# Kernel tuning notes

Hardware: AMD Instinct MI355X
Metric: run time of the kernel (lower is better)

## Reference

```python
import jax, jax.numpy as jnp
import numpy as np
from jax import lax

C = 256        # shared head channels (out_ch)
NB = 6         # anchors per spatial location
NC = 9         # num_classes (incl. background)
B = 16         # batch
FM = [(38, 38), (19, 19), (10, 10), (5, 5), (3, 3), (1, 1)]
BIAS_PRIOR = -float(np.log((1.0 - 0.01) / 0.01))  # focal-style prior on cls bias


def _conv(x, w, b):
    # 3x3 conv, stride 1, SAME padding, NCHW/OIHW
    y = lax.conv_general_dilated(x, w, (1, 1), 'SAME',
                                 dimension_numbers=('NCHW', 'OIHW', 'NCHW'))
    return y + b[None, :, None, None]


def _head(x, ws, bs):
    for w, b in zip(ws[:-1], bs[:-1]):
        x = jax.nn.relu(_conv(x, w, b))
    return _conv(x, ws[-1], bs[-1])


def setup_inputs() -> dict:
    key = jax.random.key(0)
    ks = jax.random.split(key, 20)
    d = {}
    for i, (h, w) in enumerate(FM):
        d[f'feat{i}'] = jax.random.normal(ks[i], (B, C, h, w), dtype=jnp.float32)
    for i in range(4):
        d[f'rw{i}'] = 0.01 * jax.random.normal(ks[6 + i], (C, C, 3, 3), dtype=jnp.float32)
        d[f'rb{i}'] = jnp.zeros((C,), jnp.float32)
    d['rw4'] = 0.01 * jax.random.normal(ks[10], (NB * 4, C, 3, 3), dtype=jnp.float32)
    d['rb4'] = jnp.zeros((NB * 4,), jnp.float32)
    for i in range(4):
        d[f'cw{i}'] = 0.01 * jax.random.normal(ks[11 + i], (C, C, 3, 3), dtype=jnp.float32)
        d[f'cb{i}'] = jnp.zeros((C,), jnp.float32)
    d['cw4'] = 0.01 * jax.random.normal(ks[15], (NB * NC, C, 3, 3), dtype=jnp.float32)
    cb4 = jnp.zeros((NB * NC,), jnp.float32)
    d['cb4'] = cb4.at[:NB].set(BIAS_PRIOR)  # bias_per_class = n_boxes entries
    return d


def reference(feat0, feat1, feat2, feat3, feat4, feat5,
              rw0, rw1, rw2, rw3, rw4, rb0, rb1, rb2, rb3, rb4,
              cw0, cw1, cw2, cw3, cw4, cb0, cb1, cb2, cb3, cb4):
    feats = [feat0, feat1, feat2, feat3, feat4, feat5]
    rws = [rw0, rw1, rw2, rw3, rw4]
    rbs = [rb0, rb1, rb2, rb3, rb4]
    cws = [cw0, cw1, cw2, cw3, cw4]
    cbs = [cb0, cb1, cb2, cb3, cb4]
    locs, confs = [], []
    for x in feats:
        n = x.shape[0]
        locs.append(_head(x, rws, rbs).reshape(n, 4, -1))       # [N,4,NB*H*W]
        confs.append(_head(x, cws, cbs).reshape(n, NC, -1))     # [N,NC,NB*H*W]
    bbox_delta = jnp.concatenate(locs, axis=2)   # [N, 4, total_anchors]
    confidences = jnp.concatenate(confs, axis=2)  # [N, NC, total_anchors]
    return bbox_delta, confidences
```

## Files before the change

### kernel.cpp

```cpp
#include <hip/hip_runtime.h>
#include <hip/hip_bf16.h>

typedef __attribute__((ext_vector_type(8))) __bf16 bf16x8;
typedef __attribute__((ext_vector_type(4))) float f32x4;

__device__ __forceinline__ unsigned short f2bf(float f) {
    unsigned int u = __float_as_uint(f);
    u += 0x7fff + ((u >> 16) & 1);
    return (unsigned short)(u >> 16);
}

__device__ __forceinline__ void gload16(const void* g, void* l) {
    __builtin_amdgcn_global_load_lds(
        (const __attribute__((address_space(1))) void*)g,
        (__attribute__((address_space(3))) void*)l, 16, 0, 0);
}

#define ZOFFB (31040 * 512)

__device__ __forceinline__ void tile256(int rt, int& rb, int& dim, int& row0) {
    if (rt < 91)       { rb = 0;     dim = 38; row0 = rt * 256; }
    else if (rt < 114) { rb = 23104; dim = 19; row0 = (rt - 91) * 256; }
    else if (rt < 121) { rb = 28880; dim = 10; row0 = (rt - 114) * 256; }
    else if (rt < 123) { rb = 30480; dim = 5;  row0 = (rt - 121) * 256; }
    else if (rt < 124) { rb = 30880; dim = 3;  row0 = (rt - 123) * 256; }
    else               { rb = 31024; dim = 1;  row0 = 0; }
    row0 += rb;
}

__device__ __forceinline__ void tile128(int rt, int& rb, int& dim, int& row0, int& aoff) {
    if (rt < 181)      { rb = 0;     dim = 38; row0 = rt * 128;         aoff = 0;     }
    else if (rt < 227) { rb = 23104; dim = 19; row0 = (rt - 181) * 128; aoff = 8664;  }
    else if (rt < 240) { rb = 28880; dim = 10; row0 = (rt - 227) * 128; aoff = 10830; }
    else if (rt < 244) { rb = 30480; dim = 5;  row0 = (rt - 240) * 128; aoff = 11430; }
    else if (rt < 246) { rb = 30880; dim = 3;  row0 = (rt - 244) * 128; aoff = 11580; }
    else               { rb = 31024; dim = 1;  row0 = (rt - 246) * 128; aoff = 11634; }
    row0 += rb;
}

struct WT { const float* src[10]; };
__global__ void wtrans_all(WT wt, unsigned short* __restrict__ Wb, unsigned short* __restrict__ WF) {
    int idx = blockIdx.x * 256 + threadIdx.x;
    if (idx >= 5013504) return;
    const float* src;
    unsigned short* dst;
    int lo, Cout;
    if (idx < 4718592) {
        int slot = idx / 589824;
        lo = idx - slot * 589824;
        src = wt.src[slot];
        dst = Wb + (size_t)slot * 589824;
        Cout = 256;
    } else {
        int r = idx - 4718592;
        int slot = r / 147456;
        lo = r - slot * 147456;
        src = wt.src[8 + slot];
        dst = WF + (size_t)slot * 147456;
        Cout = slot ? 54 : 24;
    }
    int co = lo / 2304;
    int k  = lo - co * 2304;
    int tap = k >> 8;
    int ci  = k & 255;
    float v = (co < Cout) ? src[(co * 256 + ci) * 9 + tap] : 0.0f;
    dst[lo] = f2bf(v);
}

struct FT { const float* src[6]; unsigned short* halo[4]; int nh; };
__global__ void ftrans_all(FT ft, unsigned short* __restrict__ X0) {
    int idx = blockIdx.x * 256 + threadIdx.x;
    if (idx >= 993280) {
        int idx2 = idx - 993280;
        int buf = idx2 >> 8, off = idx2 & 255;
        if (buf < ft.nh) ft.halo[buf][off] = 0;
        return;
    }
    int row = idx >> 5;
    int c8  = (idx & 31) << 3;
    int m, rb, dim;
    if (row < 23104)      { m = 0; rb = 0;     dim = 38; }
    else if (row < 28880) { m = 1; rb = 23104; dim = 19; }
    else if (row < 30480) { m = 2; rb = 28880; dim = 10; }
    else if (row < 30880) { m = 3; rb = 30480; dim = 5;  }
    else if (row < 31024) { m = 4; rb = 30880; dim = 3;  }
    else                  { m = 5; rb = 31024; dim = 1;  }
    int HW = dim * dim;
    int rel = row - rb;
    int b = rel / HW;
    int hw = rel - b * HW;
    const float* s = ft.src[m] + (size_t)(b * 256 + c8) * HW + hw;
    union { unsigned short u[8]; uint4 v; } tmp;
#pragma unroll
    for (int j = 0; j < 8; ++j) tmp.u[j] = f2bf(s[(size_t)j * HW]);
    *reinterpret_cast<uint4*>(X0 + ((size_t)row << 8) + c8) = tmp.v;
}

struct GArgs {
    const unsigned short* X[2];
    const unsigned short* W[2];
    const float* B[2];
    unsigned short* Y[2];
};

__global__ __launch_bounds__(512, 2) void conv_gemm(GArgs ga) {
    __shared__ unsigned char As[65536];
    __shared__ unsigned char Bs[65536];

    const int hz = blockIdx.y;
    const unsigned char* __restrict__ Xb = (const unsigned char*)ga.X[hz];
    const unsigned char* __restrict__ Wt = (const unsigned char*)ga.W[hz];
    const float* __restrict__ bias = ga.B[hz];
    unsigned short* __restrict__ Y = ga.Y[hz];

    int rb, dim, row0;
    tile256(blockIdx.x, rb, dim, row0);
    const int HWm = dim * dim;
    const int rowEnd = rb + 16 * HWm;

    const int tid = threadIdx.x;
    const int lane = tid & 63, wid = tid >> 6;
    const int lr = lane & 15, lg = lane >> 4;
    const int wm = wid >> 2, wn = wid & 3;

    const int sr0 = tid >> 2;
    const int xsw = (((tid & 3) ^ ((sr0 >> 1) & 3)) << 4);
    const unsigned char* Zr = Xb + ZOFFB + xsw;

    int gg[2], ay[2], ax[2];
    bool av[2];
#pragma unroll
    for (int it = 0; it < 2; ++it) {
        int g = row0 + sr0 + it * 128;
        bool v = g < rowEnd;
        int rel = v ? (g - rb) : 0;
        int b = rel / HWm;
        int hw = rel - b * HWm;
        int y = hw / dim;
        gg[it] = g; ay[it] = y; ax[it] = hw - y * dim; av[it] = v;
    }

    const unsigned char* bsrc0 = Wt + (size_t)sr0 * 4608 + xsw;
    const unsigned char* bsrc1 = Wt + (size_t)(sr0 + 128) * 4608 + xsw;

    auto tapA = [&](int tap, const unsigned char*& p0, const unsigned char*& p1) {
        int q3 = tap / 3;
        int dy = q3 - 1, dx = tap - q3 * 3 - 1;
        int ddd = dy * dim + dx;
        bool v0 = av[0] && ((unsigned)(ay[0] + dy) < (unsigned)dim) && ((unsigned)(ax[0] + dx) < (unsigned)dim);
        bool v1 = av[1] && ((unsigned)(ay[1] + dy) < (unsigned)dim) && ((unsigned)(ax[1] + dx) < (unsigned)dim);
        p0 = v0 ? Xb + (size_t)(gg[0] + ddd) * 512 + xsw : Zr;
        p1 = v1 ? Xb + (size_t)(gg[1] + ddd) * 512 + xsw : Zr;
    };

    const int fswz = ((lg ^ ((lr >> 1) & 3)) << 4);
    const int aRd = (wm * 128 + lr) * 64 + fswz;
    const int bRd = (wn * 64 + lr) * 64 + fswz;
    const int dSt = wid * 1024;

    f32x4 acc[8][4];
#pragma unroll
    for (int i = 0; i < 8; ++i)
#pragma unroll
        for (int j = 0; j < 4; ++j) acc[i][j] = (f32x4){0.f, 0.f, 0.f, 0.f};

    bf16x8 rA[2][8], rB[2][4];

    const unsigned char *aC0, *aC1, *aN0, *aN1;
    tapA(0, aC0, aC1);
#pragma unroll
    for (int kt = 0; kt < 3; ++kt) {
        gload16(aC0 + kt * 64, As + kt * 16384 + dSt);
        gload16(aC1 + kt * 64, As + kt * 16384 + 8192 + dSt);
        gload16(bsrc0 + kt * 64, Bs + kt * 16384 + dSt);
        gload16(bsrc1 + kt * 64, Bs + kt * 16384 + 8192 + dSt);
    }
    asm volatile("s_waitcnt vmcnt(8)" ::: "memory");
    __builtin_amdgcn_s_barrier();
#pragma unroll
    for (int i = 0; i < 8; ++i) rA[0][i] = *(const bf16x8*)(As + aRd + i * 1024);
#pragma unroll
    for (int j = 0; j < 4; ++j) rB[0][j] = *(const bf16x8*)(Bs + bRd + j * 1024);

#pragma unroll 1
    for (int tap = 0; tap < 9; ++tap) {
        if (tap < 8) tapA(tap + 1, aN0, aN1);
        else { aN0 = Zr; aN1 = Zr; }
        const unsigned char* bT0 = bsrc0 + tap * 512;
        const unsigned char* bT1 = bsrc1 + tap * 512;

#pragma unroll
        for (int kc = 0; kc < 8; ++kc) {
            const int cur = kc & 1;
            const int nslot = (kc + 1) & 3;
            const int sslot = (kc + 3) & 3;

            asm volatile("s_waitcnt vmcnt(4)" ::: "memory");
            __builtin_amdgcn_s_barrier();

            {
                const unsigned char *sa0, *sa1;
                if (kc < 5) { sa0 = aC0 + (kc + 3) * 64; sa1 = aC1 + (kc + 3) * 64; }
                else        { sa0 = aN0 + (kc - 5) * 64; sa1 = aN1 + (kc - 5) * 64; }
                gload16(sa0, As + sslot * 16384 + dSt);
                gload16(sa1, As + sslot * 16384 + 8192 + dSt);
                gload16(bT0 + (kc + 3) * 64, Bs + sslot * 16384 + dSt);
                gload16(bT1 + (kc + 3) * 64, Bs + sslot * 16384 + 8192 + dSt);
            }

#pragma unroll
            for (int i = 0; i < 8; ++i)
                rA[cur ^ 1][i] = *(const bf16x8*)(As + nslot * 16384 + aRd + i * 1024);
#pragma unroll
            for (int j = 0; j < 4; ++j)
                rB[cur ^ 1][j] = *(const bf16x8*)(Bs + nslot * 16384 + bRd + j * 1024);

            asm volatile("s_waitcnt lgkmcnt(12)" ::: "memory");
            __builtin_amdgcn_sched_barrier(0);
            __builtin_amdgcn_s_setprio(1);
#pragma unroll
            for (int i = 0; i < 8; ++i)
#pragma unroll
                for (int j = 0; j < 4; ++j)
                    acc[i][j] = __builtin_amdgcn_mfma_f32_16x16x32_bf16(rA[cur][i], rB[cur][j], acc[i][j], 0, 0, 0);
            __builtin_amdgcn_s_setprio(0);
        }
        aC0 = aN0; aC1 = aN1;
    }

    float bj[4];
#pragma unroll
    for (int j = 0; j < 4; ++j) bj[j] = bias[wn * 64 + j * 16 + lr];
#pragma unroll
    for (int i = 0; i < 8; ++i) {
        int rbase = row0 + wm * 128 + i * 16 + lg * 4;
#pragma unroll
        for (int rr = 0; rr < 4; ++rr) {
            int orow = rbase + rr;
            if (orow < rowEnd) {
                size_t yb = (size_t)orow * 256 + wn * 64 + lr;
#pragma unroll
                for (int j = 0; j < 4; ++j) {
                    float v = acc[i][j][rr] + bj[j];
                    Y[yb + j * 16] = f2bf(fmaxf(v, 0.f));
                }
            }
        }
    }
}

struct FArgs {
    const unsigned short* X[2];
    const unsigned short* W[2];
    const float* B[2];
    float* out;
    int hbase;
};

__global__ __launch_bounds__(256) void conv_final(FArgs fa) {
    __shared__ unsigned char As[2][8192];
    __shared__ unsigned char Bs[2][4096];

    const int zi = blockIdx.z;
    const int hz = zi + fa.hbase;
    const unsigned char* Xb = (const unsigned char*)fa.X[zi];
    const unsigned char* Wt = (const unsigned char*)fa.W[zi];
    const float* bias = fa.B[zi];
    float* out = fa.out;

    int rb, dim, row0, aoff;
    tile128(blockIdx.x, rb, dim, row0, aoff);
    const int HWm = dim * dim;
    const int rowEnd = rb + 16 * HWm;

    const int tid = threadIdx.x;
    const int lane = tid & 63, wid = tid >> 6;
    const int lr = lane & 15, lg = lane >> 4;

    const int swz16 = (((lane & 3) ^ ((lane >> 3) & 3)) << 4);
    const int srow = wid * 16 + (lane >> 2);

    int ay[2], ax[2], arel[2];
    bool av0[2];
#pragma unroll
    for (int it = 0; it < 2; ++it) {
        int r = row0 + it * 64 + srow;
        bool v = r < rowEnd;
        int rel = v ? (r - rb) : 0;
        int b = rel / HWm;
        int hw = rel - b * HWm;
        int y = hw / dim;
        ay[it] = y; ax[it] = hw - y * dim; arel[it] = rel; av0[it] = v;
    }

    const unsigned char* bB = Wt + (size_t)srow * 4608 + swz16;

    const int fsw = ((lg ^ ((lr >> 1) & 3)) << 4);
    const int aRd = (wid * 32 + lr) * 64 + fsw;
    const int bRd = lr * 64 + fsw;
    const int dA0 = wid * 1024;

    f32x4 acc[2][4];
#pragma unroll
    for (int i = 0; i < 2; ++i)
#pragma unroll
        for (int j = 0; j < 4; ++j) acc[i][j] = (f32x4){0.f, 0.f, 0.f, 0.f};

    auto tapPtr = [&](int tap, const unsigned char** aP) {
        int q3 = tap / 3;
        int dy = q3 - 1, dx = tap - q3 * 3 - 1;
#pragma unroll
        for (int it = 0; it < 2; ++it) {
            bool v = av0[it] && ((unsigned)(ay[it] + dy) < (unsigned)dim)
                             && ((unsigned)(ax[it] + dx) < (unsigned)dim);
            int off = v ? (rb + arel[it] + dy * dim + dx) * 512 : ZOFFB;
            aP[it] = Xb + off + swz16;
        }
    };

    const unsigned char* aP[2];
    tapPtr(0, aP);
    gload16(aP[0], &As[0][dA0]);
    gload16(aP[1], &As[0][dA0 + 4096]);
    gload16(bB, &Bs[0][dA0]);
    __syncthreads();

#pragma unroll 1
    for (int tap = 0; tap < 9; ++tap) {
        const unsigned char* aPn[2];
        if (tap < 8) tapPtr(tap + 1, aPn);
        else { aPn[0] = aP[0]; aPn[1] = aP[1]; }
        const unsigned char* bP = bB + tap * 512;

#pragma unroll
        for (int kin = 0; kin < 8; ++kin) {
            const int cur = kin & 1, nxt = cur ^ 1;
            if (kin < 7) {
                gload16(aP[0] + (kin + 1) * 64, &As[nxt][dA0]);
                gload16(aP[1] + (kin + 1) * 64, &As[nxt][dA0 + 4096]);
                gload16(bP + (kin + 1) * 64, &Bs[nxt][dA0]);
            } else if (tap < 8) {
                gload16(aPn[0], &As[nxt][dA0]);
                gload16(aPn[1], &As[nxt][dA0 + 4096]);
                gload16(bP + 512, &Bs[nxt][dA0]);
            }
            bf16x8 af[2], bg[4];
#pragma unroll
            for (int i = 0; i < 2; ++i)
                af[i] = *(const bf16x8*)(&As[cur][0] + aRd + i * 1024);
#pragma unroll
            for (int j = 0; j < 4; ++j)
                bg[j] = *(const bf16x8*)(&Bs[cur][0] + bRd + j * 1024);
#pragma unroll
            for (int i = 0; i < 2; ++i)
#pragma unroll
                for (int j = 0; j < 4; ++j)
                    acc[i][j] = __builtin_amdgcn_mfma_f32_16x16x32_bf16(af[i], bg[j], acc[i][j], 0, 0, 0);
            __syncthreads();
        }
        aP[0] = aPn[0]; aP[1] = aPn[1];
    }

    const int Cout = hz ? 54 : 24;
#pragma unroll
    for (int i = 0; i < 2; ++i) {
        int rbase = row0 + wid * 32 + i * 16 + lg * 4;
#pragma unroll
        for (int r = 0; r < 4; ++r) {
            int orow = rbase + r;
            if (orow < rowEnd) {
                int rel = orow - rb;
                int b = rel / HWm;
                int hw = rel - b * HWm;
#pragma unroll
                for (int j = 0; j < 4; ++j) {
                    int oc = j * 16 + lr;
                    if (oc < Cout) {
                        int q = oc / 6;
                        int s = oc - q * 6;
                        int anchor = aoff + s * HWm + hw;
                        float v = acc[i][j][r] + bias[oc];
                        if (hz)
                            out[744960 + (size_t)b * 104760 + (size_t)q * 11640 + anchor] = v;
                        else
                            out[(size_t)b * 46560 + (size_t)q * 11640 + anchor] = v;
                    }
                }
            }
        }
    }
}

extern "C" void kernel_launch(void* const* d_in, const int* in_sizes, int n_in,
                              void* d_out, int out_size, void* d_ws, size_t ws_size,
                              hipStream_t stream) {
    (void)in_sizes; (void)n_in; (void)out_size;

    const float* rw[5]  = {(const float*)d_in[6],  (const float*)d_in[8],
                           (const float*)d_in[10], (const float*)d_in[12],
                           (const float*)d_in[14]};
    const float* rbv[5] = {(const float*)d_in[7],  (const float*)d_in[9],
                           (const float*)d_in[11], (const float*)d_in[13],
                           (const float*)d_in[15]};
    const float* cw[5]  = {(const float*)d_in[16], (const float*)d_in[18],
                           (const float*)d_in[20], (const float*)d_in[22],
                           (const float*)d_in[24]};
    const float* cbv[5] = {(const float*)d_in[17], (const float*)d_in[19],
                           (const float*)d_in[21], (const float*)d_in[23],
                           (const float*)d_in[25]};

    const size_t ACTB = 31041ull * 512;
    const size_t WMAT = 589824;
    const size_t WBYTES = 8 * WMAT * 2;
    const size_t WFBYTES = 2 * 147456 * 2;
    const size_t needF = 4 * ACTB + WBYTES + WFBYTES;
    const size_t needS = 3 * ACTB + WBYTES + WFBYTES;

    unsigned char* ws = (unsigned char*)d_ws;
    bool fused = (ws_size >= needF);
    if (!fused && ws_size < needS) return;

    int nact = fused ? 4 : 3;
    unsigned short* act[4];
    for (int i = 0; i < nact; ++i) act[i] = (unsigned short*)(ws + (size_t)i * ACTB);
    unsigned short* Wb = (unsigned short*)(ws + (size_t)nact * ACTB);
    unsigned short* WF = (unsigned short*)(ws + (size_t)nact * ACTB + WBYTES);

    WT wt;
    for (int l = 0; l < 4; ++l) { wt.src[l] = rw[l]; wt.src[4 + l] = cw[l]; }
    wt.src[8] = rw[4]; wt.src[9] = cw[4];
    wtrans_all<<<19584, 256, 0, stream>>>(wt, Wb, WF);

    FT ft;
    for (int i = 0; i < 6; ++i) ft.src[i] = (const float*)d_in[i];
    for (int i = 0; i < 4; ++i)
        ft.halo[i] = (unsigned short*)((unsigned char*)act[i < nact ? i : 0] + ZOFFB);
    ft.nh = nact;
    ftrans_all<<<3884, 256, 0, stream>>>(ft, act[0]);

    const unsigned short* Wr[5], *Wc[5];
    for (int l = 0; l < 4; ++l) {
        Wr[l] = Wb + (size_t)l * WMAT;
        Wc[l] = Wb + (size_t)(4 + l) * WMAT;
    }
    Wr[4] = WF; Wc[4] = WF + 147456;

    if (fused) {
        unsigned short* X0 = act[0];
        unsigned short* P = act[1];
        unsigned short* Q = act[2];
        unsigned short* R = act[3];
        GArgs l1 = {{X0, X0}, {Wr[0], Wc[0]}, {rbv[0], cbv[0]}, {P, Q}};
        GArgs l2 = {{P,  Q},  {Wr[1], Wc[1]}, {rbv[1], cbv[1]}, {X0, R}};
        GArgs l3 = {{X0, R},  {Wr[2], Wc[2]}, {rbv[2], cbv[2]}, {P, Q}};
        GArgs l4 = {{P,  Q},  {Wr[3], Wc[3]}, {rbv[3], cbv[3]}, {X0, R}};
        conv_gemm<<<dim3(125, 2), 512, 0, stream>>>(l1);
        conv_gemm<<<dim3(125, 2), 512, 0, stream>>>(l2);
        conv_gemm<<<dim3(125, 2), 512, 0, stream>>>(l3);
        conv_gemm<<<dim3(125, 2), 512, 0, stream>>>(l4);
        FArgs lf = {{X0, R}, {Wr[4], Wc[4]}, {rbv[4], cbv[4]}, (float*)d_out, 0};
        conv_final<<<dim3(247, 1, 2), 256, 0, stream>>>(lf);
    } else {
        unsigned short* X0 = act[0];
        unsigned short* A1 = act[1];
        unsigned short* A2 = act[2];
        for (int h = 0; h < 2; ++h) {
            const unsigned short* const* W = h ? Wc : Wr;
            const float* const* bs = h ? cbv : rbv;
            GArgs l1 = {{X0, X0}, {W[0], W[0]}, {bs[0], bs[0]}, {A1, A1}};
            GArgs l2 = {{A1, A1}, {W[1], W[1]}, {bs[1], bs[1]}, {A2, A2}};
            GArgs l3 = {{A2, A2}, {W[2], W[2]}, {bs[2], bs[2]}, {A1, A1}};
            GArgs l4 = {{A1, A1}, {W[3], W[3]}, {bs[3], bs[3]}, {A2, A2}};
            conv_gemm<<<dim3(125, 1), 512, 0, stream>>>(l1);
            conv_gemm<<<dim3(125, 1), 512, 0, stream>>>(l2);
            conv_gemm<<<dim3(125, 1), 512, 0, stream>>>(l3);
            conv_gemm<<<dim3(125, 1), 512, 0, stream>>>(l4);
            FArgs lf = {{A2, A2}, {W[4], W[4]}, {bs[4], bs[4]}, (float*)d_out, h};
            conv_final<<<dim3(247, 1, 1), 256, 0, stream>>>(lf);
        }
    }
}
```

Baseline: 418.0 us.

## Split conv GEMM tiles along N with XCD-aware block mapping and 3-stage pipeline

Changes the conv GEMM block tile from 256x256 (512 threads) to 256x128 (256 threads), giving 500 blocks instead of 250. Block IDs are remapped so that neighbouring tiles of the same head land on the same XCD, which should improve L2 sharing of the activation rows loaded by both N-halves. The LDS pipeline shrinks to a 3-slot ring with a deeper prefetch distance, and the register double-buffering of MFMA fragments is replaced by a full lgkmcnt wait. The intent is better CU occupancy and load balance, at the cost of reloading A tiles twice and less overlap of LDS reads with MFMA work.

```diff
diff --git a/kernel.cpp b/kernel.cpp
--- a/kernel.cpp
+++ b/kernel.cpp
@@ -103,60 +103,89 @@
     unsigned short* Y[2];
 };
 
-__global__ __launch_bounds__(512, 2) void conv_gemm(GArgs ga) {
-    __shared__ unsigned char As[65536];
-    __shared__ unsigned char Bs[65536];
-
-    const int hz = blockIdx.y;
+__global__ __launch_bounds__(256, 2) void conv_gemm(GArgs ga) {
+    __shared__ unsigned char As[49152];
+    __shared__ unsigned char Bs[24576];
+
+    const int bid = blockIdx.x;
+    const int xcd = bid & 7, sub = bid >> 3;
+    const int d = (xcd < 4) ? (xcd * 63 + sub) : (252 + (xcd - 4) * 62 + sub);
+    const int hz = (d >= 250) ? 1 : 0;
+    const int rr = d - (hz ? 250 : 0);
+    const int rt = rr >> 1, nt = rr & 1;
+
     const unsigned char* __restrict__ Xb = (const unsigned char*)ga.X[hz];
     const unsigned char* __restrict__ Wt = (const unsigned char*)ga.W[hz];
     const float* __restrict__ bias = ga.B[hz];
     unsigned short* __restrict__ Y = ga.Y[hz];
 
     int rb, dim, row0;
-    tile256(blockIdx.x, rb, dim, row0);
+    tile256(rt, rb, dim, row0);
     const int HWm = dim * dim;
     const int rowEnd = rb + 16 * HWm;
+    const int n0 = nt * 128;
 
     const int tid = threadIdx.x;
     const int lane = tid & 63, wid = tid >> 6;
     const int lr = lane & 15, lg = lane >> 4;
-    const int wm = wid >> 2, wn = wid & 3;
-
-    const int sr0 = tid >> 2;
-    const int xsw = (((tid & 3) ^ ((sr0 >> 1) & 3)) << 4);
+    const int wm = wid >> 1, wn = wid & 1;
+
+    const int tq = tid & 3;
+    const int trow = tid >> 2;
+    const int xsw = ((tq ^ ((trow >> 1) & 3)) << 4);
     const unsigned char* Zr = Xb + ZOFFB + xsw;
 
-    int gg[2], ay[2], ax[2];
-    bool av[2];
-#pragma unroll
-    for (int it = 0; it < 2; ++it) {
-        int g = row0 + sr0 + it * 128;
+    int gg[4], ayy[4], axx[4];
+    bool av[4];
+#pragma unroll
+    for (int k = 0; k < 4; ++k) {
+        int g = row0 + trow + 64 * k;
         bool v = g < rowEnd;
         int rel = v ? (g - rb) : 0;
         int b = rel / HWm;
         int hw = rel - b * HWm;
         int y = hw / dim;
-        gg[it] = g; ay[it] = y; ax[it] = hw - y * dim; av[it] = v;
-    }
-
-    const unsigned char* bsrc0 = Wt + (size_t)sr0 * 4608 + xsw;
-    const unsigned char* bsrc1 = Wt + (size_t)(sr0 + 128) * 4608 + xsw;
-
-    auto tapA = [&](int tap, const unsigned char*& p0, const unsigned char*& p1) {
+        gg[k] = g; ayy[k] = y; axx[k] = hw - y * dim; av[k] = v;
+    }
+
+    const unsigned char* bsrc0 = Wt + (size_t)(n0 + trow) * 4608 + xsw;
+
+    auto tapA = [&](int tap, const unsigned char** p) {
         int q3 = tap / 3;
         int dy = q3 - 1, dx = tap - q3 * 3 - 1;
         int ddd = dy * dim + dx;
-        bool v0 = av[0] && ((unsigned)(ay[0] + dy) < (unsigned)dim) && ((unsigned)(ax[0] + dx) < (unsigned)dim);
-        bool v1 = av[1] && ((unsigned)(ay[1] + dy) < (unsigned)dim) && ((unsigned)(ax[1] + dx) < (unsigned)dim);
-        p0 = v0 ? Xb + (size_t)(gg[0] + ddd) * 512 + xsw : Zr;
-        p1 = v1 ? Xb + (size_t)(gg[1] + ddd) * 512 + xsw : Zr;
+#pragma unroll
+        for (int k = 0; k < 4; ++k) {
+            bool v = av[k] && ((unsigned)(ayy[k] + dy) < (unsigned)dim)
+                           && ((unsigned)(axx[k] + dx) < (unsigned)dim);
+            p[k] = v ? Xb + (size_t)(gg[k] + ddd) * 512 + xsw : Zr;
+        }
+    };
+
+    unsigned char* AsB = &As[0];
+    unsigned char* BsB = &Bs[0];
+    auto STAGE = [&](const unsigned char* const* pA, const unsigned char* bT, int kk, int sl) {
+        int off = kk * 64;
+        unsigned char* ad = AsB + sl * 16384 + wid * 1024;
+        unsigned char* bd = BsB + sl * 8192 + wid * 1024;
+        gload16(pA[0] + off, ad);
+        gload16(pA[1] + off, ad + 4096);
+        gload16(pA[2] + off, ad + 8192);
+        gload16(pA[3] + off, ad + 12288);
+        gload16(bT + off, bd);
+        gload16(bT + 294912 + off, bd + 4096);
+    };
+    auto STAGEZ = [&](int sl) {
+        unsigned char* ad = AsB + sl * 16384 + wid * 1024;
+        unsigned char* bd = BsB + sl * 8192 + wid * 1024;
+        gload16(Zr, ad); gload16(Zr, ad + 4096);
+        gload16(Zr, ad + 8192); gload16(Zr, ad + 12288);
+        gload16(Zr, bd); gload16(Zr, bd + 4096);
     };
 
     const int fswz = ((lg ^ ((lr >> 1) & 3)) << 4);
     const int aRd = (wm * 128 + lr) * 64 + fswz;
     const int bRd = (wn * 64 + lr) * 64 + fswz;
-    const int dSt = wid * 1024;
 
     f32x4 acc[8][4];
 #pragma unroll
@@ -164,84 +193,70 @@
 #pragma unroll
         for (int j = 0; j < 4; ++j) acc[i][j] = (f32x4){0.f, 0.f, 0.f, 0.f};
 
-    bf16x8 rA[2][8], rB[2][4];
-
-    const unsigned char *aC0, *aC1, *aN0, *aN1;
-    tapA(0, aC0, aC1);
-#pragma unroll
-    for (int kt = 0; kt < 3; ++kt) {
-        gload16(aC0 + kt * 64, As + kt * 16384 + dSt);
-        gload16(aC1 + kt * 64, As + kt * 16384 + 8192 + dSt);
-        gload16(bsrc0 + kt * 64, Bs + kt * 16384 + dSt);
-        gload16(bsrc1 + kt * 64, Bs + kt * 16384 + 8192 + dSt);
-    }
-    asm volatile("s_waitcnt vmcnt(8)" ::: "memory");
-    __builtin_amdgcn_s_barrier();
-#pragma unroll
-    for (int i = 0; i < 8; ++i) rA[0][i] = *(const bf16x8*)(As + aRd + i * 1024);
-#pragma unroll
-    for (int j = 0; j < 4; ++j) rB[0][j] = *(const bf16x8*)(Bs + bRd + j * 1024);
+    const unsigned char* aS[4];
+    tapA(0, aS);
+    STAGE(aS, bsrc0, 0, 0);
+    STAGE(aS, bsrc0, 1, 1);
+
+    int cs = 0, ss = 2;
 
 #pragma unroll 1
     for (int tap = 0; tap < 9; ++tap) {
-        if (tap < 8) tapA(tap + 1, aN0, aN1);
-        else { aN0 = Zr; aN1 = Zr; }
-        const unsigned char* bT0 = bsrc0 + tap * 512;
-        const unsigned char* bT1 = bsrc1 + tap * 512;
+        const unsigned char* aN[4];
+        if (tap < 8) tapA(tap + 1, aN);
+        else { aN[0] = aN[1] = aN[2] = aN[3] = Zr; }
+        const unsigned char* bC = bsrc0 + tap * 512;
+        const unsigned char* bN = bsrc0 + (tap < 8 ? (tap + 1) * 512 : 0);
 
 #pragma unroll
         for (int kc = 0; kc < 8; ++kc) {
-            const int cur = kc & 1;
-            const int nslot = (kc + 1) & 3;
-            const int sslot = (kc + 3) & 3;
-
-            asm volatile("s_waitcnt vmcnt(4)" ::: "memory");
+            asm volatile("s_waitcnt vmcnt(6)" ::: "memory");
             __builtin_amdgcn_s_barrier();
 
-            {
-                const unsigned char *sa0, *sa1;
-                if (kc < 5) { sa0 = aC0 + (kc + 3) * 64; sa1 = aC1 + (kc + 3) * 64; }
-                else        { sa0 = aN0 + (kc - 5) * 64; sa1 = aN1 + (kc - 5) * 64; }
-                gload16(sa0, As + sslot * 16384 + dSt);
-                gload16(sa1, As + sslot * 16384 + 8192 + dSt);
-                gload16(bT0 + (kc + 3) * 64, Bs + sslot * 16384 + dSt);
-                gload16(bT1 + (kc + 3) * 64, Bs + sslot * 16384 + 8192 + dSt);
-            }
-
+            if (kc < 6)           STAGE(aS, bC, kc + 2, ss);
+            else if (tap < 8)     STAGE(aN, bN, kc - 6, ss);
+            else                  STAGEZ(ss);
+
+            bf16x8 rA[8], rB[4];
+            const unsigned char* ab = AsB + cs * 16384;
+            const unsigned char* bb = BsB + cs * 8192;
 #pragma unroll
             for (int i = 0; i < 8; ++i)
-                rA[cur ^ 1][i] = *(const bf16x8*)(As + nslot * 16384 + aRd + i * 1024);
+                rA[i] = *(const bf16x8*)(ab + aRd + i * 1024);
 #pragma unroll
             for (int j = 0; j < 4; ++j)
-                rB[cur ^ 1][j] = *(const bf16x8*)(Bs + nslot * 16384 + bRd + j * 1024);
-
-            asm volatile("s_waitcnt lgkmcnt(12)" ::: "memory");
+                rB[j] = *(const bf16x8*)(bb + bRd + j * 1024);
+            asm volatile("s_waitcnt lgkmcnt(0)" ::: "memory");
             __builtin_amdgcn_sched_barrier(0);
+
             __builtin_amdgcn_s_setprio(1);
 #pragma unroll
             for (int i = 0; i < 8; ++i)
 #pragma unroll
                 for (int j = 0; j < 4; ++j)
-                    acc[i][j] = __builtin_amdgcn_mfma_f32_16x16x32_bf16(rA[cur][i], rB[cur][j], acc[i][j], 0, 0, 0);
+                    acc[i][j] = __builtin_amdgcn_mfma_f32_16x16x32_bf16(rA[i], rB[j], acc[i][j], 0, 0, 0);
             __builtin_amdgcn_s_setprio(0);
-        }
-        aC0 = aN0; aC1 = aN1;
+
+            cs = (cs == 2) ? 0 : cs + 1;
+            ss = (ss == 2) ? 0 : ss + 1;
+        }
+        aS[0] = aN[0]; aS[1] = aN[1]; aS[2] = aN[2]; aS[3] = aN[3];
     }
 
     float bj[4];
 #pragma unroll
-    for (int j = 0; j < 4; ++j) bj[j] = bias[wn * 64 + j * 16 + lr];
+    for (int j = 0; j < 4; ++j) bj[j] = bias[n0 + wn * 64 + j * 16 + lr];
 #pragma unroll
     for (int i = 0; i < 8; ++i) {
         int rbase = row0 + wm * 128 + i * 16 + lg * 4;
 #pragma unroll
-        for (int rr = 0; rr < 4; ++rr) {
-            int orow = rbase + rr;
+        for (int rr2 = 0; rr2 < 4; ++rr2) {
+            int orow = rbase + rr2;
             if (orow < rowEnd) {
-                size_t yb = (size_t)orow * 256 + wn * 64 + lr;
+                size_t yb = (size_t)orow * 256 + n0 + wn * 64 + lr;
 #pragma unroll
                 for (int j = 0; j < 4; ++j) {
-                    float v = acc[i][j][rr] + bj[j];
+                    float v = acc[i][j][rr2] + bj[j];
                     Y[yb + j * 16] = f2bf(fmaxf(v, 0.f));
                 }
             }
@@ -454,10 +469,10 @@
         GArgs l2 = {{P,  Q},  {Wr[1], Wc[1]}, {rbv[1], cbv[1]}, {X0, R}};
         GArgs l3 = {{X0, R},  {Wr[2], Wc[2]}, {rbv[2], cbv[2]}, {P, Q}};
         GArgs l4 = {{P,  Q},  {Wr[3], Wc[3]}, {rbv[3], cbv[3]}, {X0, R}};
-        conv_gemm<<<dim3(125, 2), 512, 0, stream>>>(l1);
-        conv_gemm<<<dim3(125, 2), 512, 0, stream>>>(l2);
-        conv_gemm<<<dim3(125, 2), 512, 0, stream>>>(l3);
-        conv_gemm<<<dim3(125, 2), 512, 0, stream>>>(l4);
+        conv_gemm<<<500, 256, 0, stream>>>(l1);
+        conv_gemm<<<500, 256, 0, stream>>>(l2);
+        conv_gemm<<<500, 256, 0, stream>>>(l3);
+        conv_gemm<<<500, 256, 0, stream>>>(l4);
         FArgs lf = {{X0, R}, {Wr[4], Wc[4]}, {rbv[4], cbv[4]}, (float*)d_out, 0};
         conv_final<<<dim3(247, 1, 2), 256, 0, stream>>>(lf);
     } else {
@@ -471,10 +486,10 @@
             GArgs l2 = {{A1, A1}, {W[1], W[1]}, {bs[1], bs[1]}, {A2, A2}};
             GArgs l3 = {{A2, A2}, {W[2], W[2]}, {bs[2], bs[2]}, {A1, A1}};
             GArgs l4 = {{A1, A1}, {W[3], W[3]}, {bs[3], bs[3]}, {A2, A2}};
-            conv_gemm<<<dim3(125, 1), 512, 0, stream>>>(l1);
-            conv_gemm<<<dim3(125, 1), 512, 0, stream>>>(l2);
-            conv_gemm<<<dim3(125, 1), 512, 0, stream>>>(l3);
-            conv_gemm<<<dim3(125, 1), 512, 0, stream>>>(l4);
+            conv_gemm<<<500, 256, 0, stream>>>(l1);
+            conv_gemm<<<500, 256, 0, stream>>>(l2);
+            conv_gemm<<<500, 256, 0, stream>>>(l3);
+            conv_gemm<<<500, 256, 0, stream>>>(l4);
             FArgs lf = {{A2, A2}, {W[4], W[4]}, {bs[4], bs[4]}, (float*)d_out, h};
             conv_final<<<dim3(247, 1, 1), 256, 0, stream>>>(lf);
         }
```

Result: slower. 476.9 us (+14.1%).

## Retile conv GEMM to 128x256 tiles with 32x32 MFMA and 3-stage LDS ring

Applied to the files above, without the earlier changes.

The implicit-GEMM conv kernel moves from 256x256 output tiles with 16x16x32 MFMAs to 128-row tiles with 32x32x16 MFMAs. It uses a 3-slot unified LDS ring of 72KB and raises launch bounds to target more resident blocks. The grid roughly doubles (247 tiles) to fill the CUs better on the uneven per-level row counts. The trade-off is less reuse of each weight tile per block and a shallower prefetch depth, in exchange for better occupancy, load balance and fewer accumulator registers.

```diff
diff --git a/kernel.cpp b/kernel.cpp
--- a/kernel.cpp
+++ b/kernel.cpp
@@ -3,6 +3,7 @@
 
 typedef __attribute__((ext_vector_type(8))) __bf16 bf16x8;
 typedef __attribute__((ext_vector_type(4))) float f32x4;
+typedef __attribute__((ext_vector_type(16))) float f32x16;
 
 __device__ __forceinline__ unsigned short f2bf(float f) {
     unsigned int u = __float_as_uint(f);
@@ -17,16 +18,6 @@
 }
 
 #define ZOFFB (31040 * 512)
-
-__device__ __forceinline__ void tile256(int rt, int& rb, int& dim, int& row0) {
-    if (rt < 91)       { rb = 0;     dim = 38; row0 = rt * 256; }
-    else if (rt < 114) { rb = 23104; dim = 19; row0 = (rt - 91) * 256; }
-    else if (rt < 121) { rb = 28880; dim = 10; row0 = (rt - 114) * 256; }
-    else if (rt < 123) { rb = 30480; dim = 5;  row0 = (rt - 121) * 256; }
-    else if (rt < 124) { rb = 30880; dim = 3;  row0 = (rt - 123) * 256; }
-    else               { rb = 31024; dim = 1;  row0 = 0; }
-    row0 += rb;
-}
 
 __device__ __forceinline__ void tile128(int rt, int& rb, int& dim, int& row0, int& aoff) {
     if (rt < 181)      { rb = 0;     dim = 38; row0 = rt * 128;         aoff = 0;     }
@@ -103,9 +94,8 @@
     unsigned short* Y[2];
 };
 
-__global__ __launch_bounds__(512, 2) void conv_gemm(GArgs ga) {
-    __shared__ unsigned char As[65536];
-    __shared__ unsigned char Bs[65536];
+__global__ __launch_bounds__(512, 4) void conv_gemm(GArgs ga) {
+    __shared__ unsigned char Ls[73728];
 
     const int hz = blockIdx.y;
     const unsigned char* __restrict__ Xb = (const unsigned char*)ga.X[hz];
@@ -113,136 +103,132 @@
     const float* __restrict__ bias = ga.B[hz];
     unsigned short* __restrict__ Y = ga.Y[hz];
 
-    int rb, dim, row0;
-    tile256(blockIdx.x, rb, dim, row0);
+    int rb, dim, row0, aoff;
+    tile128(blockIdx.x, rb, dim, row0, aoff);
     const int HWm = dim * dim;
     const int rowEnd = rb + 16 * HWm;
 
     const int tid = threadIdx.x;
     const int lane = tid & 63, wid = tid >> 6;
-    const int lr = lane & 15, lg = lane >> 4;
+    const int l31 = lane & 31, lh = lane >> 5;
     const int wm = wid >> 2, wn = wid & 3;
 
-    const int sr0 = tid >> 2;
-    const int xsw = (((tid & 3) ^ ((sr0 >> 1) & 3)) << 4);
+    const int tq = tid & 3;
+    const int srow = tid >> 2;
+    const int xsw = ((tq ^ ((srow >> 1) & 3)) << 4);
     const unsigned char* Zr = Xb + ZOFFB + xsw;
 
-    int gg[2], ay[2], ax[2];
-    bool av[2];
-#pragma unroll
-    for (int it = 0; it < 2; ++it) {
-        int g = row0 + sr0 + it * 128;
-        bool v = g < rowEnd;
-        int rel = v ? (g - rb) : 0;
-        int b = rel / HWm;
-        int hw = rel - b * HWm;
-        int y = hw / dim;
-        gg[it] = g; ay[it] = y; ax[it] = hw - y * dim; av[it] = v;
-    }
-
-    const unsigned char* bsrc0 = Wt + (size_t)sr0 * 4608 + xsw;
-    const unsigned char* bsrc1 = Wt + (size_t)(sr0 + 128) * 4608 + xsw;
-
-    auto tapA = [&](int tap, const unsigned char*& p0, const unsigned char*& p1) {
+    const int g = row0 + srow;
+    const bool avv = g < rowEnd;
+    int rel = avv ? (g - rb) : 0;
+    int bb_ = rel / HWm;
+    int hw = rel - bb_ * HWm;
+    int ay = hw / dim;
+    int ax = hw - ay * dim;
+
+    const unsigned char* bsrc = Wt + (size_t)srow * 4608 + xsw;
+
+    auto tapA = [&](int tap) -> const unsigned char* {
         int q3 = tap / 3;
         int dy = q3 - 1, dx = tap - q3 * 3 - 1;
-        int ddd = dy * dim + dx;
-        bool v0 = av[0] && ((unsigned)(ay[0] + dy) < (unsigned)dim) && ((unsigned)(ax[0] + dx) < (unsigned)dim);
-        bool v1 = av[1] && ((unsigned)(ay[1] + dy) < (unsigned)dim) && ((unsigned)(ax[1] + dx) < (unsigned)dim);
-        p0 = v0 ? Xb + (size_t)(gg[0] + ddd) * 512 + xsw : Zr;
-        p1 = v1 ? Xb + (size_t)(gg[1] + ddd) * 512 + xsw : Zr;
+        bool v = avv && ((unsigned)(ay + dy) < (unsigned)dim) && ((unsigned)(ax + dx) < (unsigned)dim);
+        return v ? Xb + (size_t)(g + dy * dim + dx) * 512 + xsw : Zr;
     };
 
-    const int fswz = ((lg ^ ((lr >> 1) & 3)) << 4);
-    const int aRd = (wm * 128 + lr) * 64 + fswz;
-    const int bRd = (wn * 64 + lr) * 64 + fswz;
-    const int dSt = wid * 1024;
-
-    f32x4 acc[8][4];
-#pragma unroll
-    for (int i = 0; i < 8; ++i)
-#pragma unroll
-        for (int j = 0; j < 4; ++j) acc[i][j] = (f32x4){0.f, 0.f, 0.f, 0.f};
-
-    bf16x8 rA[2][8], rB[2][4];
-
-    const unsigned char *aC0, *aC1, *aN0, *aN1;
-    tapA(0, aC0, aC1);
-#pragma unroll
-    for (int kt = 0; kt < 3; ++kt) {
-        gload16(aC0 + kt * 64, As + kt * 16384 + dSt);
-        gload16(aC1 + kt * 64, As + kt * 16384 + 8192 + dSt);
-        gload16(bsrc0 + kt * 64, Bs + kt * 16384 + dSt);
-        gload16(bsrc1 + kt * 64, Bs + kt * 16384 + 8192 + dSt);
-    }
-    asm volatile("s_waitcnt vmcnt(8)" ::: "memory");
-    __builtin_amdgcn_s_barrier();
-#pragma unroll
-    for (int i = 0; i < 8; ++i) rA[0][i] = *(const bf16x8*)(As + aRd + i * 1024);
-#pragma unroll
-    for (int j = 0; j < 4; ++j) rB[0][j] = *(const bf16x8*)(Bs + bRd + j * 1024);
+    const int dA = wid * 1024;
+    const int dB = 24576 + wid * 1024;
+
+    auto STAGE = [&](const unsigned char* aP, const unsigned char* bT, int kk, int sA_, int sB_) {
+        gload16(aP + kk * 64, Ls + sA_ + dA);
+        gload16(bT + kk * 64, Ls + sB_ + dB);
+        gload16(bT + 589824 + kk * 64, Ls + sB_ + dB + 8192);
+    };
+
+    const int ar = wm * 64 + l31;
+    const int rA0 = ar * 64 + (((0 + lh) ^ ((ar >> 1) & 3)) << 4);
+    const int rA1 = ar * 64 + (((2 + lh) ^ ((ar >> 1) & 3)) << 4);
+    const int cb = wn * 64 + l31;
+    const int rB0 = 24576 + cb * 64 + (((0 + lh) ^ ((cb >> 1) & 3)) << 4);
+    const int rB1 = 24576 + cb * 64 + (((2 + lh) ^ ((cb >> 1) & 3)) << 4);
+
+    f32x16 acc[2][2];
+#pragma unroll
+    for (int i = 0; i < 2; ++i)
+#pragma unroll
+        for (int j = 0; j < 2; ++j) acc[i][j] = (f32x16){0.f};
+
+    const unsigned char* aC = tapA(0);
+    STAGE(aC, bsrc, 0, 0, 0);
+    STAGE(aC, bsrc, 1, 8192, 16384);
+    int cA = 0, cB = 0;
+    int sA = 16384, sB = 32768;
 
 #pragma unroll 1
     for (int tap = 0; tap < 9; ++tap) {
-        if (tap < 8) tapA(tap + 1, aN0, aN1);
-        else { aN0 = Zr; aN1 = Zr; }
-        const unsigned char* bT0 = bsrc0 + tap * 512;
-        const unsigned char* bT1 = bsrc1 + tap * 512;
+        const unsigned char* aN = (tap < 8) ? tapA(tap + 1) : Zr;
+        const unsigned char* bT = bsrc + tap * 512;
 
 #pragma unroll
         for (int kc = 0; kc < 8; ++kc) {
-            const int cur = kc & 1;
-            const int nslot = (kc + 1) & 3;
-            const int sslot = (kc + 3) & 3;
-
-            asm volatile("s_waitcnt vmcnt(4)" ::: "memory");
+            asm volatile("s_waitcnt vmcnt(3)" ::: "memory");
             __builtin_amdgcn_s_barrier();
 
-            {
-                const unsigned char *sa0, *sa1;
-                if (kc < 5) { sa0 = aC0 + (kc + 3) * 64; sa1 = aC1 + (kc + 3) * 64; }
-                else        { sa0 = aN0 + (kc - 5) * 64; sa1 = aN1 + (kc - 5) * 64; }
-                gload16(sa0, As + sslot * 16384 + dSt);
-                gload16(sa1, As + sslot * 16384 + 8192 + dSt);
-                gload16(bT0 + (kc + 3) * 64, Bs + sslot * 16384 + dSt);
-                gload16(bT1 + (kc + 3) * 64, Bs + sslot * 16384 + 8192 + dSt);
-            }
-
-#pragma unroll
-            for (int i = 0; i < 8; ++i)
-                rA[cur ^ 1][i] = *(const bf16x8*)(As + nslot * 16384 + aRd + i * 1024);
-#pragma unroll
-            for (int j = 0; j < 4; ++j)
-                rB[cur ^ 1][j] = *(const bf16x8*)(Bs + nslot * 16384 + bRd + j * 1024);
-
-            asm volatile("s_waitcnt lgkmcnt(12)" ::: "memory");
+            if (tap == 8 && kc >= 6) {
+                gload16(Zr, Ls + sA + dA);
+                gload16(Zr, Ls + sB + dB);
+                gload16(Zr, Ls + sB + dB + 8192);
+            } else if (kc < 6) {
+                STAGE(aC, bT, kc + 2, sA, sB);
+            } else {
+                STAGE(aN, bT + 512, kc - 6, sA, sB);
+            }
+
+            bf16x8 af[2][2], bf[2][2];
+#pragma unroll
+            for (int i = 0; i < 2; ++i) {
+                af[i][0] = *(const bf16x8*)(Ls + cA + rA0 + i * 2048);
+                af[i][1] = *(const bf16x8*)(Ls + cA + rA1 + i * 2048);
+            }
+#pragma unroll
+            for (int j = 0; j < 2; ++j) {
+                bf[j][0] = *(const bf16x8*)(Ls + cB + rB0 + j * 2048);
+                bf[j][1] = *(const bf16x8*)(Ls + cB + rB1 + j * 2048);
+            }
+            asm volatile("s_waitcnt lgkmcnt(0)" ::: "memory");
             __builtin_amdgcn_sched_barrier(0);
             __builtin_amdgcn_s_setprio(1);
 #pragma unroll
-            for (int i = 0; i < 8; ++i)
-#pragma unroll
-                for (int j = 0; j < 4; ++j)
-                    acc[i][j] = __builtin_amdgcn_mfma_f32_16x16x32_bf16(rA[cur][i], rB[cur][j], acc[i][j], 0, 0, 0);
+            for (int kf = 0; kf < 2; ++kf)
+#pragma unroll
+                for (int i = 0; i < 2; ++i)
+#pragma unroll
+                    for (int j = 0; j < 2; ++j)
+                        acc[i][j] = __builtin_amdgcn_mfma_f32_32x32x16_bf16(af[i][kf], bf[j][kf], acc[i][j], 0, 0, 0);
             __builtin_amdgcn_s_setprio(0);
-        }
-        aC0 = aN0; aC1 = aN1;
-    }
-
-    float bj[4];
-#pragma unroll
-    for (int j = 0; j < 4; ++j) bj[j] = bias[wn * 64 + j * 16 + lr];
-#pragma unroll
-    for (int i = 0; i < 8; ++i) {
-        int rbase = row0 + wm * 128 + i * 16 + lg * 4;
-#pragma unroll
-        for (int rr = 0; rr < 4; ++rr) {
-            int orow = rbase + rr;
+
+            cA = (cA == 16384) ? 0 : cA + 8192;
+            sA = (sA == 16384) ? 0 : sA + 8192;
+            cB = (cB == 32768) ? 0 : cB + 16384;
+            sB = (sB == 32768) ? 0 : sB + 16384;
+        }
+        aC = aN;
+    }
+
+    float bj[2];
+#pragma unroll
+    for (int j = 0; j < 2; ++j) bj[j] = bias[wn * 64 + j * 32 + l31];
+#pragma unroll
+    for (int i = 0; i < 2; ++i) {
+        int rbase = row0 + wm * 64 + i * 32 + 4 * lh;
+#pragma unroll
+        for (int q = 0; q < 16; ++q) {
+            int orow = rbase + (q & 3) + 8 * (q >> 2);
             if (orow < rowEnd) {
-                size_t yb = (size_t)orow * 256 + wn * 64 + lr;
-#pragma unroll
-                for (int j = 0; j < 4; ++j) {
-                    float v = acc[i][j][rr] + bj[j];
-                    Y[yb + j * 16] = f2bf(fmaxf(v, 0.f));
+                size_t yb = (size_t)orow * 256 + wn * 64 + l31;
+#pragma unroll
+                for (int j = 0; j < 2; ++j) {
+                    float v = acc[i][j][q] + bj[j];
+                    Y[yb + j * 32] = f2bf(fmaxf(v, 0.f));
                 }
             }
         }
@@ -454,10 +440,10 @@
         GArgs l2 = {{P,  Q},  {Wr[1], Wc[1]}, {rbv[1], cbv[1]}, {X0, R}};
         GArgs l3 = {{X0, R},  {Wr[2], Wc[2]}, {rbv[2], cbv[2]}, {P, Q}};
         GArgs l4 = {{P,  Q},  {Wr[3], Wc[3]}, {rbv[3], cbv[3]}, {X0, R}};
-        conv_gemm<<<dim3(125, 2), 512, 0, stream>>>(l1);
-        conv_gemm<<<dim3(125, 2), 512, 0, stream>>>(l2);
-        conv_gemm<<<dim3(125, 2), 512, 0, stream>>>(l3);
-        conv_gemm<<<dim3(125, 2), 512, 0, stream>>>(l4);
+        conv_gemm<<<dim3(247, 2), 512, 0, stream>>>(l1);
+        conv_gemm<<<dim3(247, 2), 512, 0, stream>>>(l2);
+        conv_gemm<<<dim3(247, 2), 512, 0, stream>>>(l3);
+        conv_gemm<<<dim3(247, 2), 512, 0, stream>>>(l4);
         FArgs lf = {{X0, R}, {Wr[4], Wc[4]}, {rbv[4], cbv[4]}, (float*)d_out, 0};
         conv_final<<<dim3(247, 1, 2), 256, 0, stream>>>(lf);
     } else {
@@ -471,10 +457,10 @@
             GArgs l2 = {{A1, A1}, {W[1], W[1]}, {bs[1], bs[1]}, {A2, A2}};
             GArgs l3 = {{A2, A2}, {W[2], W[2]}, {bs[2], bs[2]}, {A1, A1}};
             GArgs l4 = {{A1, A1}, {W[3], W[3]}, {bs[3], bs[3]}, {A2, A2}};
-            conv_gemm<<<dim3(125, 1), 512, 0, stream>>>(l1);
-            conv_gemm<<<dim3(125, 1), 512, 0, stream>>>(l2);
-            conv_gemm<<<dim3(125, 1), 512, 0, stream>>>(l3);
-            conv_gemm<<<dim3(125, 1), 512, 0, stream>>>(l4);
+            conv_gemm<<<dim3(247, 1), 512, 0, stream>>>(l1);
+            conv_gemm<<<dim3(247, 1), 512, 0, stream>>>(l2);
+            conv_gemm<<<dim3(247, 1), 512, 0, stream>>>(l3);
+            conv_gemm<<<dim3(247, 1), 512, 0, stream>>>(l4);
             FArgs lf = {{A2, A2}, {W[4], W[4]}, {bs[4], bs[4]}, (float*)d_out, h};
             conv_final<<<dim3(247, 1, 1), 256, 0, stream>>>(lf);
         }
```

Result: slower. 470.9 us (+12.6%).

## Load conv activations directly into registers and reorder loop to tap-inner

Applied to the files above, without the earlier changes.

Drops the shared-memory staging buffer for the im2col activation operand. Each lane now reads its A fragments straight from global memory into registers, with per-row tap bounds checks. The loop order changes from tap-outer/channel-chunk-inner to channel-chunk-outer/tap-inner, and only the weight tile still goes through a 4-slot LDS ring. This halves LDS use and removes the A-side LDS writes and reads, at the cost of more scattered global loads and more registers per thread, which could expose memory latency.

```diff
diff --git a/kernel.cpp b/kernel.cpp
--- a/kernel.cpp
+++ b/kernel.cpp
@@ -104,7 +104,6 @@
 };
 
 __global__ __launch_bounds__(512, 2) void conv_gemm(GArgs ga) {
-    __shared__ unsigned char As[65536];
     __shared__ unsigned char Bs[65536];
 
     const int hz = blockIdx.y;
@@ -123,40 +122,31 @@
     const int lr = lane & 15, lg = lane >> 4;
     const int wm = wid >> 2, wn = wid & 3;
 
-    const int sr0 = tid >> 2;
-    const int xsw = (((tid & 3) ^ ((sr0 >> 1) & 3)) << 4);
-    const unsigned char* Zr = Xb + ZOFFB + xsw;
-
-    int gg[2], ay[2], ax[2];
-    bool av[2];
-#pragma unroll
-    for (int it = 0; it < 2; ++it) {
-        int g = row0 + sr0 + it * 128;
-        bool v = g < rowEnd;
-        int rel = v ? (g - rb) : 0;
+    const int sr0 = tid >> 2, tq = tid & 3;
+    const int xsw = ((tq ^ ((sr0 >> 1) & 3)) << 4);
+    const unsigned char* bsrc0 = Wt + (size_t)sr0 * 4608 + xsw;
+    const unsigned char* bsrc1 = Wt + (size_t)(sr0 + 128) * 4608 + xsw;
+    const int dSt = wid * 1024;
+    unsigned char* BsP = &Bs[0];
+
+    const int fswz = ((lg ^ ((lr >> 1) & 3)) << 4);
+    const int bRd = (wn * 64 + lr) * 64 + fswz;
+
+    const unsigned char* zPtr = Xb + ZOFFB + lg * 16;
+    const unsigned char* aBase[8];
+    int ay8[8], ax8[8];
+    bool rv8[8];
+#pragma unroll
+    for (int i = 0; i < 8; ++i) {
+        int r = row0 + wm * 128 + i * 16 + lr;
+        bool v = r < rowEnd;
+        int rel = v ? (r - rb) : 0;
         int b = rel / HWm;
         int hw = rel - b * HWm;
         int y = hw / dim;
-        gg[it] = g; ay[it] = y; ax[it] = hw - y * dim; av[it] = v;
-    }
-
-    const unsigned char* bsrc0 = Wt + (size_t)sr0 * 4608 + xsw;
-    const unsigned char* bsrc1 = Wt + (size_t)(sr0 + 128) * 4608 + xsw;
-
-    auto tapA = [&](int tap, const unsigned char*& p0, const unsigned char*& p1) {
-        int q3 = tap / 3;
-        int dy = q3 - 1, dx = tap - q3 * 3 - 1;
-        int ddd = dy * dim + dx;
-        bool v0 = av[0] && ((unsigned)(ay[0] + dy) < (unsigned)dim) && ((unsigned)(ax[0] + dx) < (unsigned)dim);
-        bool v1 = av[1] && ((unsigned)(ay[1] + dy) < (unsigned)dim) && ((unsigned)(ax[1] + dx) < (unsigned)dim);
-        p0 = v0 ? Xb + (size_t)(gg[0] + ddd) * 512 + xsw : Zr;
-        p1 = v1 ? Xb + (size_t)(gg[1] + ddd) * 512 + xsw : Zr;
-    };
-
-    const int fswz = ((lg ^ ((lr >> 1) & 3)) << 4);
-    const int aRd = (wm * 128 + lr) * 64 + fswz;
-    const int bRd = (wn * 64 + lr) * 64 + fswz;
-    const int dSt = wid * 1024;
+        rv8[i] = v; ay8[i] = y; ax8[i] = hw - y * dim;
+        aBase[i] = Xb + (size_t)(rb + rel) * 512 + lg * 16;
+    }
 
     f32x4 acc[8][4];
 #pragma unroll
@@ -164,69 +154,79 @@
 #pragma unroll
         for (int j = 0; j < 4; ++j) acc[i][j] = (f32x4){0.f, 0.f, 0.f, 0.f};
 
-    bf16x8 rA[2][8], rB[2][4];
-
-    const unsigned char *aC0, *aC1, *aN0, *aN1;
-    tapA(0, aC0, aC1);
-#pragma unroll
-    for (int kt = 0; kt < 3; ++kt) {
-        gload16(aC0 + kt * 64, As + kt * 16384 + dSt);
-        gload16(aC1 + kt * 64, As + kt * 16384 + 8192 + dSt);
-        gload16(bsrc0 + kt * 64, Bs + kt * 16384 + dSt);
-        gload16(bsrc1 + kt * 64, Bs + kt * 16384 + 8192 + dSt);
-    }
-    asm volatile("s_waitcnt vmcnt(8)" ::: "memory");
-    __builtin_amdgcn_s_barrier();
-#pragma unroll
-    for (int i = 0; i < 8; ++i) rA[0][i] = *(const bf16x8*)(As + aRd + i * 1024);
-#pragma unroll
-    for (int j = 0; j < 4; ++j) rB[0][j] = *(const bf16x8*)(Bs + bRd + j * 1024);
+    bf16x8 aR0[8], aR1[8];
+
+    gload16(bsrc0, BsP + dSt);
+    gload16(bsrc1, BsP + dSt + 8192);
+    gload16(bsrc0 + 512, BsP + 16384 + dSt);
+    gload16(bsrc1 + 512, BsP + 16384 + dSt + 8192);
+    gload16(bsrc0 + 1024, BsP + 32768 + dSt);
+    gload16(bsrc1 + 1024, BsP + 32768 + dSt + 8192);
+    __builtin_amdgcn_sched_barrier(0);
+#pragma unroll
+    for (int i = 0; i < 8; ++i) {
+        bool v = rv8[i] && ((unsigned)(ay8[i] - 1) < (unsigned)dim)
+                        && ((unsigned)(ax8[i] - 1) < (unsigned)dim);
+        const unsigned char* p = v ? (aBase[i] + (ptrdiff_t)(-dim - 1) * 512) : zPtr;
+        aR0[i] = *(const bf16x8*)p;
+    }
+    __builtin_amdgcn_sched_barrier(0);
+
+    int cs = 0, ss = 49152;
+
+#define STEP(AC, AN, TAP, KCV) do {                                             \
+    asm volatile("s_waitcnt vmcnt(12)" ::: "memory");                           \
+    __builtin_amdgcn_s_barrier();                                               \
+    {   const int stap = ((TAP) + 3 <= 8) ? ((TAP) + 3) : ((TAP) - 6);          \
+        const int skc  = ((TAP) + 3 <= 8) ? (KCV) : ((KCV) + 1);                \
+        const unsigned char* b0 = bsrc0 + stap * 512 + skc * 64;                \
+        const unsigned char* b1 = bsrc1 + stap * 512 + skc * 64;                \
+        gload16(b0, BsP + ss + dSt);                                            \
+        gload16(b1, BsP + ss + dSt + 8192);                                     \
+    }                                                                           \
+    __builtin_amdgcn_sched_barrier(0);                                          \
+    {   const int ntap = ((TAP) + 1 <= 8) ? ((TAP) + 1) : 0;                    \
+        const int nkc  = ((TAP) + 1 <= 8) ? (KCV) : ((KCV) + 1);                \
+        const int q3 = ntap / 3;                                                \
+        const int dyn = q3 - 1, dxn = ntap - q3 * 3 - 1;                        \
+        const ptrdiff_t sOff = (ptrdiff_t)(dyn * dim + dxn) * 512 + nkc * 64;   \
+        _Pragma("unroll")                                                       \
+        for (int i = 0; i < 8; ++i) {                                           \
+            bool v = rv8[i] && ((unsigned)(ay8[i] + dyn) < (unsigned)dim)       \
+                            && ((unsigned)(ax8[i] + dxn) < (unsigned)dim);      \
+            const unsigned char* p = v ? (aBase[i] + sOff) : zPtr;              \
+            AN[i] = *(const bf16x8*)p;                                          \
+        }                                                                       \
+    }                                                                           \
+    bf16x8 bf_[4];                                                              \
+    _Pragma("unroll")                                                           \
+    for (int j = 0; j < 4; ++j)                                                 \
+        bf_[j] = *(const bf16x8*)(BsP + cs + bRd + j * 1024);                   \
+    asm volatile("s_waitcnt vmcnt(10) lgkmcnt(0)" ::: "memory");                \
+    __builtin_amdgcn_sched_barrier(0);                                          \
+    __builtin_amdgcn_s_setprio(1);                                              \
+    _Pragma("unroll")                                                           \
+    for (int i = 0; i < 8; ++i)                                                 \
+        _Pragma("unroll")                                                       \
+        for (int j = 0; j < 4; ++j)                                             \
+            acc[i][j] = __builtin_amdgcn_mfma_f32_16x16x32_bf16(AC[i], bf_[j],  \
+                                                                acc[i][j], 0, 0, 0); \
+    __builtin_amdgcn_s_setprio(0);                                              \
+    cs = (cs + 16384) & 65535;                                                  \
+    ss = (ss + 16384) & 65535;                                                  \
+} while (0)
 
 #pragma unroll 1
-    for (int tap = 0; tap < 9; ++tap) {
-        if (tap < 8) tapA(tap + 1, aN0, aN1);
-        else { aN0 = Zr; aN1 = Zr; }
-        const unsigned char* bT0 = bsrc0 + tap * 512;
-        const unsigned char* bT1 = bsrc1 + tap * 512;
-
-#pragma unroll
-        for (int kc = 0; kc < 8; ++kc) {
-            const int cur = kc & 1;
-            const int nslot = (kc + 1) & 3;
-            const int sslot = (kc + 3) & 3;
-
-            asm volatile("s_waitcnt vmcnt(4)" ::: "memory");
-            __builtin_amdgcn_s_barrier();
-
-            {
-                const unsigned char *sa0, *sa1;
-                if (kc < 5) { sa0 = aC0 + (kc + 3) * 64; sa1 = aC1 + (kc + 3) * 64; }
-                else        { sa0 = aN0 + (kc - 5) * 64; sa1 = aN1 + (kc - 5) * 64; }
-                gload16(sa0, As + sslot * 16384 + dSt);
-                gload16(sa1, As + sslot * 16384 + 8192 + dSt);
-                gload16(bT0 + (kc + 3) * 64, Bs + sslot * 16384 + dSt);
-                gload16(bT1 + (kc + 3) * 64, Bs + sslot * 16384 + 8192 + dSt);
-            }
-
-#pragma unroll
-            for (int i = 0; i < 8; ++i)
-                rA[cur ^ 1][i] = *(const bf16x8*)(As + nslot * 16384 + aRd + i * 1024);
-#pragma unroll
-            for (int j = 0; j < 4; ++j)
-                rB[cur ^ 1][j] = *(const bf16x8*)(Bs + nslot * 16384 + bRd + j * 1024);
-
-            asm volatile("s_waitcnt lgkmcnt(12)" ::: "memory");
-            __builtin_amdgcn_sched_barrier(0);
-            __builtin_amdgcn_s_setprio(1);
-#pragma unroll
-            for (int i = 0; i < 8; ++i)
-#pragma unroll
-                for (int j = 0; j < 4; ++j)
-                    acc[i][j] = __builtin_amdgcn_mfma_f32_16x16x32_bf16(rA[cur][i], rB[cur][j], acc[i][j], 0, 0, 0);
-            __builtin_amdgcn_s_setprio(0);
-        }
-        aC0 = aN0; aC1 = aN1;
-    }
+    for (int kc2 = 0; kc2 < 4; ++kc2) {
+        const int k0 = kc2 * 2, k1 = kc2 * 2 + 1;
+        STEP(aR0, aR1, 0, k0); STEP(aR1, aR0, 1, k0); STEP(aR0, aR1, 2, k0);
+        STEP(aR1, aR0, 3, k0); STEP(aR0, aR1, 4, k0); STEP(aR1, aR0, 5, k0);
+        STEP(aR0, aR1, 6, k0); STEP(aR1, aR0, 7, k0); STEP(aR0, aR1, 8, k0);
+        STEP(aR1, aR0, 0, k1); STEP(aR0, aR1, 1, k1); STEP(aR1, aR0, 2, k1);
+        STEP(aR0, aR1, 3, k1); STEP(aR1, aR0, 4, k1); STEP(aR0, aR1, 5, k1);
+        STEP(aR1, aR0, 6, k1); STEP(aR0, aR1, 7, k1); STEP(aR1, aR0, 8, k1);
+    }
+#undef STEP
 
     float bj[4];
 #pragma unroll
```

Result: slower. 983.0 us (+135.2%).
